# Kernel optimization log

Measured on AMD Instinct MI355X. Metric: run time of the kernel, lower is better.

The kernel has to match this reference:

```python
import jax, jax.numpy as jnp
import numpy as np

K = 3  # kernel size
PAD = K // 2


def setup_inputs() -> dict:
    key = jax.random.key(0)
    k1, k2, k3 = jax.random.split(key, 3)
    B, C, H, W = 8, 192, 128, 128
    x = jax.random.normal(k1, (B, C, H, W), dtype=jnp.float32)
    kernel = 0.02 * jax.random.normal(k2, (C, K * K), dtype=jnp.float32)
    gate_w = 0.02 * jax.random.normal(k3, (C,), dtype=jnp.float32)
    gate_b = jnp.zeros((C,), dtype=jnp.float32)
    return {"x": x, "kernel": kernel, "gate_w": gate_w, "gate_b": gate_b}


def reference(x, kernel, gate_w, gate_b):
    B, C, H, W = x.shape
    # F.unfold with zero padding: patches[b,c,ki*K+kj,h,w] = x_pad[b,c,h+ki,w+kj]
    xp = jnp.pad(x, ((0, 0), (0, 0), (PAD, PAD), (PAD, PAD)))
    patches = jnp.stack(
        [xp[:, :, i:i + H, j:j + W] for i in range(K) for j in range(K)],
        axis=2,
    )  # [B, C, K*K, H, W]
    # depthwise 1x1 gate: per-channel scale + bias, then sigmoid
    theta = jax.nn.sigmoid(x * gate_w[None, :, None, None] + gate_b[None, :, None, None])
    # max-plus: max_v [ f(u-v) + theta(u) * k(v) ]
    scored = patches + theta[:, :, None] * kernel[None, :, :, None, None]
    return jnp.max(scored, axis=2)  # [B, C, H, W]
```

## Files before the change

### kernel.cpp

```cpp
#include <hip/hip_runtime.h>
#include <math.h>

#define BB 8
#define CC 192
#define HH 128
#define WW 128
#define IMGF (HH * WW)
#define NWAVE 6144
#define NSTEP 4

typedef float vf4 __attribute__((ext_vector_type(4)));

__device__ __forceinline__ float col9(float a0, float a1, float a2,
                                      float b0, float b1, float b2,
                                      float c0, float c1, float c2,
                                      float th, const float* kk) {
    float m;
    m = fmaf(th, kk[0], a0);
    m = fmaxf(m, fmaf(th, kk[1], a1));
    m = fmaxf(m, fmaf(th, kk[2], a2));
    m = fmaxf(m, fmaf(th, kk[3], b0));
    m = fmaxf(m, fmaf(th, kk[4], b1));
    m = fmaxf(m, fmaf(th, kk[5], b2));
    m = fmaxf(m, fmaf(th, kk[6], c0));
    m = fmaxf(m, fmaf(th, kk[7], c1));
    m = fmaxf(m, fmaf(th, kk[8], c2));
    return m;
}

__global__ __launch_bounds__(256) void dynmorph_kernel(
    const float* __restrict__ x,
    const float* __restrict__ kern,
    const float* __restrict__ gw,
    const float* __restrict__ gb,
    float* __restrict__ out)
{
    const int tid  = threadIdx.x;
    const int lane = tid & 63;
    const int wg   = lane & 31;
    const int hf   = lane >> 5;
    const int col  = wg * 4;
    const int wv   = __builtin_amdgcn_readfirstlane((int)(threadIdx.x >> 6));
    const int w    = blockIdx.x * 4 + wv;

#pragma unroll
    for (int s = 0; s < NSTEP; ++s) {
        const int p   = s * NWAVE + w;
        const int bc  = p >> 4;
        const int c   = bc % CC;
        const int ir0 = ((p & 15) << 3) + (hf << 2);

        const float* xb = x   + (size_t)bc * IMGF;
        float*       ob = out + (size_t)bc * IMGF;

        float kk[9];
#pragma unroll
        for (int i = 0; i < 9; ++i) kk[i] = kern[c * 9 + i];
        const float gwc = gw[c];
        const float gbc = gb[c];

        vf4 buf[6];
#pragma unroll
        for (int j = 0; j < 6; ++j) {
            const int lr = ir0 - 1 + j;
            buf[j] = (lr >= 0 && lr < HH) ? *(const vf4*)(xb + lr * WW + col)
                                          : (vf4)(0.0f);
        }

        float lf[6], rt[6];
#pragma unroll
        for (int j = 0; j < 6; ++j) {
            const float l = __shfl_up(buf[j].w, 1);
            const float r = __shfl_down(buf[j].x, 1);
            lf[j] = (wg == 0)  ? 0.0f : l;
            rt[j] = (wg == 31) ? 0.0f : r;
        }

#pragma unroll
        for (int j = 0; j < 4; ++j) {
            const vf4 A  = buf[j];
            const vf4 B  = buf[j + 1];
            const vf4 Cv = buf[j + 2];

            const float t0 = __builtin_amdgcn_rcpf(1.0f + __expf(-fmaf(B.x, gwc, gbc)));
            const float t1 = __builtin_amdgcn_rcpf(1.0f + __expf(-fmaf(B.y, gwc, gbc)));
            const float t2 = __builtin_amdgcn_rcpf(1.0f + __expf(-fmaf(B.z, gwc, gbc)));
            const float t3 = __builtin_amdgcn_rcpf(1.0f + __expf(-fmaf(B.w, gwc, gbc)));

            vf4 o;
            o.x = col9(lf[j],     A.x, A.y,
                       lf[j + 1], B.x, B.y,
                       lf[j + 2], Cv.x, Cv.y, t0, kk);
            o.y = col9(A.x, A.y, A.z,
                       B.x, B.y, B.z,
                       Cv.x, Cv.y, Cv.z, t1, kk);
            o.z = col9(A.y, A.z, A.w,
                       B.y, B.z, B.w,
                       Cv.y, Cv.z, Cv.w, t2, kk);
            o.w = col9(A.z, A.w, rt[j],
                       B.z, B.w, rt[j + 1],
                       Cv.z, Cv.w, rt[j + 2], t3, kk);

            *(vf4*)(ob + (ir0 + j) * WW + col) = o;
        }
    }
}

extern "C" void kernel_launch(void* const* d_in, const int* in_sizes, int n_in,
                              void* d_out, int out_size, void* d_ws, size_t ws_size,
                              hipStream_t stream) {
    const float* x    = (const float*)d_in[0];
    const float* kern = (const float*)d_in[1];
    const float* gw   = (const float*)d_in[2];
    const float* gb   = (const float*)d_in[3];
    float* out        = (float*)d_out;

    dim3 grid(BB * CC);
    dim3 block(256);
    dynmorph_kernel<<<grid, block, 0, stream>>>(x, kern, gw, gb, out);
}
```

Baseline: 181.5 us.

## Switch to flat grid-stride mapping with one output row-segment per thread

Each thread now handles one float4 of output per iteration in a flat grid-stride loop over 2048 blocks, loading its own row plus the rows above and below directly. Previously each half-wave held a 6-row register window to produce 4 output rows, reusing vertical neighbours. The new layout issues about three loads per output vector instead of 1.5, leaning on cache for reuse, in exchange for simpler indexing and fully contiguous coalesced accesses across the wave.

```diff
diff --git a/kernel.cpp b/kernel.cpp
--- a/kernel.cpp
+++ b/kernel.cpp
@@ -5,9 +5,11 @@
 #define CC 192
 #define HH 128
 #define WW 128
-#define IMGF (HH * WW)
-#define NWAVE 6144
-#define NSTEP 4
+#define NV4   (BB * CC * HH * WW / 4)
+#define NBLK  2048
+#define NTHR  (NBLK * 256)
+#define NIT   (NV4 / NTHR)
+
 
 typedef float vf4 __attribute__((ext_vector_type(4)));
 
@@ -38,71 +40,55 @@
     const int tid  = threadIdx.x;
     const int lane = tid & 63;
     const int wg   = lane & 31;
-    const int hf   = lane >> 5;
-    const int col  = wg * 4;
-    const int wv   = __builtin_amdgcn_readfirstlane((int)(threadIdx.x >> 6));
-    const int w    = blockIdx.x * 4 + wv;
+
+    int i = blockIdx.x * 256 + tid;
 
 #pragma unroll
-    for (int s = 0; s < NSTEP; ++s) {
-        const int p   = s * NWAVE + w;
-        const int bc  = p >> 4;
-        const int c   = bc % CC;
-        const int ir0 = ((p & 15) << 3) + (hf << 2);
-
-        const float* xb = x   + (size_t)bc * IMGF;
-        float*       ob = out + (size_t)bc * IMGF;
+    for (int k = 0; k < NIT; ++k, i += NTHR) {
+        const int c = __builtin_amdgcn_readfirstlane((i >> 12) % CC);
+        const int r = (i >> 5) & (HH - 1);
 
         float kk[9];
 #pragma unroll
-        for (int i = 0; i < 9; ++i) kk[i] = kern[c * 9 + i];
+        for (int q = 0; q < 9; ++q) kk[q] = kern[c * 9 + q];
         const float gwc = gw[c];
         const float gbc = gb[c];
 
-        vf4 buf[6];
-#pragma unroll
-        for (int j = 0; j < 6; ++j) {
-            const int lr = ir0 - 1 + j;
-            buf[j] = (lr >= 0 && lr < HH) ? *(const vf4*)(xb + lr * WW + col)
-                                          : (vf4)(0.0f);
-        }
+        const float* p = x + ((size_t)i << 2);
+        const vf4 Bv = *(const vf4*)p;
+        const vf4 A  = (r > 0)      ? *(const vf4*)(p - WW) : (vf4)(0.0f);
+        const vf4 Cv = (r < HH - 1) ? *(const vf4*)(p + WW) : (vf4)(0.0f);
 
-        float lf[6], rt[6];
-#pragma unroll
-        for (int j = 0; j < 6; ++j) {
-            const float l = __shfl_up(buf[j].w, 1);
-            const float r = __shfl_down(buf[j].x, 1);
-            lf[j] = (wg == 0)  ? 0.0f : l;
-            rt[j] = (wg == 31) ? 0.0f : r;
-        }
+        const float aL0 = __shfl_up(A.w, 1),  aR0 = __shfl_down(A.x, 1);
+        const float bL0 = __shfl_up(Bv.w, 1), bR0 = __shfl_down(Bv.x, 1);
+        const float cL0 = __shfl_up(Cv.w, 1), cR0 = __shfl_down(Cv.x, 1);
+        const float aL = (wg == 0)  ? 0.0f : aL0;
+        const float bL = (wg == 0)  ? 0.0f : bL0;
+        const float cL = (wg == 0)  ? 0.0f : cL0;
+        const float aR = (wg == 31) ? 0.0f : aR0;
+        const float bR = (wg == 31) ? 0.0f : bR0;
+        const float cR = (wg == 31) ? 0.0f : cR0;
 
-#pragma unroll
-        for (int j = 0; j < 4; ++j) {
-            const vf4 A  = buf[j];
-            const vf4 B  = buf[j + 1];
-            const vf4 Cv = buf[j + 2];
+        const float t0 = __builtin_amdgcn_rcpf(1.0f + __expf(-fmaf(Bv.x, gwc, gbc)));
+        const float t1 = __builtin_amdgcn_rcpf(1.0f + __expf(-fmaf(Bv.y, gwc, gbc)));
+        const float t2 = __builtin_amdgcn_rcpf(1.0f + __expf(-fmaf(Bv.z, gwc, gbc)));
+        const float t3 = __builtin_amdgcn_rcpf(1.0f + __expf(-fmaf(Bv.w, gwc, gbc)));
 
-            const float t0 = __builtin_amdgcn_rcpf(1.0f + __expf(-fmaf(B.x, gwc, gbc)));
-            const float t1 = __builtin_amdgcn_rcpf(1.0f + __expf(-fmaf(B.y, gwc, gbc)));
-            const float t2 = __builtin_amdgcn_rcpf(1.0f + __expf(-fmaf(B.z, gwc, gbc)));
-            const float t3 = __builtin_amdgcn_rcpf(1.0f + __expf(-fmaf(B.w, gwc, gbc)));
+        vf4 o;
+        o.x = col9(aL,   A.x,  A.y,
+                   bL,   Bv.x, Bv.y,
+                   cL,   Cv.x, Cv.y, t0, kk);
+        o.y = col9(A.x,  A.y,  A.z,
+                   Bv.x, Bv.y, Bv.z,
+                   Cv.x, Cv.y, Cv.z, t1, kk);
+        o.z = col9(A.y,  A.z,  A.w,
+                   Bv.y, Bv.z, Bv.w,
+                   Cv.y, Cv.z, Cv.w, t2, kk);
+        o.w = col9(A.z,  A.w,  aR,
+                   Bv.z, Bv.w, bR,
+                   Cv.z, Cv.w, cR, t3, kk);
 
-            vf4 o;
-            o.x = col9(lf[j],     A.x, A.y,
-                       lf[j + 1], B.x, B.y,
-                       lf[j + 2], Cv.x, Cv.y, t0, kk);
-            o.y = col9(A.x, A.y, A.z,
-                       B.x, B.y, B.z,
-                       Cv.x, Cv.y, Cv.z, t1, kk);
-            o.z = col9(A.y, A.z, A.w,
-                       B.y, B.z, B.w,
-                       Cv.y, Cv.z, Cv.w, t2, kk);
-            o.w = col9(A.z, A.w, rt[j],
-                       B.z, B.w, rt[j + 1],
-                       Cv.z, Cv.w, rt[j + 2], t3, kk);
-
-            *(vf4*)(ob + (ir0 + j) * WW + col) = o;
-        }
+        *(vf4*)(out + ((size_t)i << 2)) = o;
     }
 }
 
@@ -115,7 +101,7 @@
     const float* gb   = (const float*)d_in[3];
     float* out        = (float*)d_out;
 
-    dim3 grid(BB * CC);
+    dim3 grid(NBLK);
     dim3 block(256);
     dynmorph_kernel<<<grid, block, 0, stream>>>(x, kern, gw, gb, out);
 }
```

Result: no change. 182.9 us (+0.8%).
